# Performance work log

Measured on AMD Instinct MI355X. Metric: run time of the kernel, lower is better.

Reference implementation:

```python
import jax, jax.numpy as jnp
import numpy as np
from jax import lax

B = 32      # point clouds per batch
P = 1024    # points per cloud (equal-sized, contiguous in batch vector)
K = 20      # kNN neighbors (includes self, as in PyG knn)
N = B * P


def _w(key, fan_in, fan_out):
    return jax.random.normal(key, (fan_in, fan_out), dtype=jnp.float32) / np.sqrt(fan_in)


def setup_inputs() -> dict:
    key = jax.random.key(0)
    ks = jax.random.split(key, 12)
    return {
        "pos": jax.random.normal(ks[0], (N, 3), dtype=jnp.float32),
        "batch": jnp.repeat(jnp.arange(B, dtype=jnp.int32), P),
        # conv1 MLP([6,64,64]): Linear(6,64)+BN+ReLU, Linear(64,64) plain
        "conv1_W1": _w(ks[1], 6, 64),
        "conv1_b1": jnp.zeros((64,), jnp.float32),
        "conv1_bn_scale": jnp.ones((64,), jnp.float32),   # BN eval folded affine
        "conv1_bn_bias": jnp.zeros((64,), jnp.float32),
        "conv1_W2": _w(ks[2], 64, 64),
        "conv1_b2": jnp.zeros((64,), jnp.float32),
        # conv2 MLP([128,128]): single plain Linear(128,128)
        "conv2_W": _w(ks[3], 128, 128),
        "conv2_b": jnp.zeros((128,), jnp.float32),
        # lin: Linear(64+128, 128)
        "lin_W": _w(ks[4], 192, 128),
        "lin_b": jnp.zeros((128,), jnp.float32),
    }


def _edge_conv(x, mlp_fn):
    # x: [B, P, d]. Dynamic kNN in feature space per cloud, edge MLP, max-aggregate.
    sq = jnp.sum(x * x, axis=-1)                                  # [B,P]
    dist = sq[:, :, None] - 2.0 * jnp.einsum('bpd,bqd->bpq', x, x) + sq[:, None, :]
    _, idx = lax.top_k(-dist, K)                                  # [B,P,K] nearest (incl. self)
    x_j = jax.vmap(lambda xb, ib: xb[ib])(x, idx)                 # [B,P,K,d] gather neighbors
    x_i = jnp.broadcast_to(x[:, :, None, :], x_j.shape)
    e = jnp.concatenate([x_i, x_j - x_i], axis=-1)                # [B,P,K,2d]
    return jnp.max(mlp_fn(e), axis=2)                             # max aggregation -> [B,P,out]


def reference(pos, batch, conv1_W1, conv1_b1, conv1_bn_scale, conv1_bn_bias,
              conv1_W2, conv1_b2, conv2_W, conv2_b, lin_W, lin_b):
    x = pos.reshape(B, P, 3)

    def mlp1(e):
        h = e @ conv1_W1 + conv1_b1
        h = jax.nn.relu(h * conv1_bn_scale + conv1_bn_bias)       # BN(eval) + ReLU
        return h @ conv1_W2 + conv1_b2                            # plain last layer

    def mlp2(e):
        return e @ conv2_W + conv2_b                              # plain single layer

    x1 = _edge_conv(x, mlp1)                                      # [B,P,64]
    x2 = _edge_conv(x1, mlp2)                                     # [B,P,128]
    h = jnp.concatenate([x1, x2], axis=-1) @ lin_W + lin_b        # [B,P,128]
    # global_max_pool over each cloud via batch ids
    out = jax.ops.segment_max(h.reshape(N, 128), batch, num_segments=B)
    return out                                                    # [B,128]
```

## Files before the change

### kernel.cpp

```cpp
#include <hip/hip_runtime.h>
#include <math.h>

#define NPTS 32768
#define NB 32
#define PP 1024
#define KK 20

using bf16x8 = __attribute__((ext_vector_type(8))) short;
using f32x4 = __attribute__((ext_vector_type(4))) float;

constexpr size_t OFF_X1 = 0;
constexpr size_t OFF_IDX = OFF_X1 + (size_t)NPTS * 64 * 4;
constexpr size_t OFF_U = OFF_IDX + (size_t)NPTS * KK * 4;
constexpr size_t OFF_V = OFF_U + (size_t)NPTS * 128 * 4;
constexpr size_t OFF_X2 = OFF_V + (size_t)NPTS * 128 * 4;
constexpr size_t OFF_H = OFF_X2 + (size_t)NPTS * 128 * 4;
constexpr size_t OFF_PART = OFF_H + (size_t)NPTS * 128 * 4;
constexpr size_t OFF_SQN = OFF_PART + (size_t)32 * 8 * 128 * 4;

__device__ __forceinline__ void topk_insert(unsigned (&l)[KK], unsigned key) {
#pragma unroll
  for (int j = KK - 1; j >= 1; --j) {
    unsigned r;
    asm("v_med3_u32 %0, %1, %2, %3" : "=v"(r) : "v"(key), "v"(l[j - 1]), "v"(l[j]));
    l[j] = r;
  }
  l[0] = key < l[0] ? key : l[0];
}

__device__ __forceinline__ unsigned pack_key(float dist, int q) {
  return (__float_as_uint(dist) & 0xFFFFFC00u) | (unsigned)q;
}

__device__ __forceinline__ void split_bf16(float x, short& hi, short& lo) {
  unsigned u = __float_as_uint(x);
  hi = (short)(u >> 16);
  float fh = __uint_as_float(u & 0xFFFF0000u);
  float r = x - fh;
  lo = (short)(__float_as_uint(r) >> 16);
}

template <int S>
__global__ __launch_bounds__(256) void knn_topk3(const float* __restrict__ x,
                                                 unsigned* __restrict__ pk) {
  constexpr int CH = PP / S;
  __shared__ __align__(16) float xs[1024];
  __shared__ __align__(16) float ys[1024];
  __shared__ __align__(16) float zs[1024];
  int bx = blockIdx.x;
  int s = bx % S;
  int tile = (bx / S) % (PP / 256);
  int b = bx / (S * (PP / 256));
  int tid = threadIdx.x;
  const float* xb = x + (size_t)b * PP * 3;

  for (int t = tid; t < 768; t += 256) {
    float4 v = ((const float4*)xb)[t];
    int e = 4 * t;
    float vals[4] = {v.x, v.y, v.z, v.w};
#pragma unroll
    for (int j = 0; j < 4; ++j) {
      int p = (e + j) / 3, d = (e + j) % 3;
      if (d == 0) xs[p] = vals[j];
      else if (d == 1) ys[p] = vals[j];
      else zs[p] = vals[j];
    }
  }
  __syncthreads();

  int i = tile * 256 + tid;
  float xi0 = xs[i], xi1 = ys[i], xi2 = zs[i];

  unsigned l[KK];
#pragma unroll
  for (int j = 0; j < KK; ++j) l[j] = 0xFFFFFFFFu;

  int q0 = s * CH;
  float4 qx = *(const float4*)&xs[q0];
  float4 qy = *(const float4*)&ys[q0];
  float4 qz = *(const float4*)&zs[q0];
  for (int c = 0; c < CH; c += 4) {
    int qm = (q0 + c + 4) & 1023;
    float4 nqx = *(const float4*)&xs[qm];
    float4 nqy = *(const float4*)&ys[qm];
    float4 nqz = *(const float4*)&zs[qm];
    float cx[4] = {qx.x, qx.y, qx.z, qx.w};
    float cy[4] = {qy.x, qy.y, qy.z, qy.w};
    float cz[4] = {qz.x, qz.y, qz.z, qz.w};
#pragma unroll
    for (int j = 0; j < 4; ++j) {
      float d0 = xi0 - cx[j], d1 = xi1 - cy[j], d2 = xi2 - cz[j];
      float dist = fmaf(d0, d0, fmaf(d1, d1, d2 * d2));
      topk_insert(l, pack_key(dist, q0 + c + j));
    }
    qx = nqx; qy = nqy; qz = nqz;
  }
  size_t base = ((size_t)b * PP + i) * S + s;
#pragma unroll
  for (int j = 0; j < KK; ++j) pk[base * KK + j] = l[j];
}

template <int S>
__global__ __launch_bounds__(256) void knn_merge(const unsigned* __restrict__ pk,
                                                 int* __restrict__ idx_out) {
  int p = blockIdx.x * 256 + threadIdx.x;
  const unsigned* g = pk + (size_t)p * S * KK;
  unsigned l[KK];
#pragma unroll
  for (int j = 0; j < KK; ++j) l[j] = g[j];
  for (int s = 1; s < S; ++s) {
    const unsigned* gs = g + s * KK;
#pragma unroll
    for (int j = 0; j < KK; ++j) topk_insert(l, gs[j]);
  }
#pragma unroll
  for (int j = 0; j < KK; ++j) idx_out[(size_t)p * KK + j] = (int)(l[j] & 1023u);
}

__global__ __launch_bounds__(256) void precompute1(const float* __restrict__ pos,
                                                   const float* __restrict__ W1,
                                                   const float* __restrict__ b1,
                                                   float* __restrict__ u1,
                                                   float* __restrict__ v1) {
  int gid = blockIdx.x * 256 + threadIdx.x;
  int i = gid >> 6, c = gid & 63;
  float p0 = pos[(size_t)i * 3 + 0], p1 = pos[(size_t)i * 3 + 1], p2 = pos[(size_t)i * 3 + 2];
  float a0 = W1[0 * 64 + c], a1 = W1[1 * 64 + c], a2 = W1[2 * 64 + c];
  float g0 = W1[3 * 64 + c], g1 = W1[4 * 64 + c], g2 = W1[5 * 64 + c];
  float v = fmaf(p0, g0, fmaf(p1, g1, p2 * g2));
  float u = b1[c];
  u = fmaf(p0, a0 - g0, u);
  u = fmaf(p1, a1 - g1, u);
  u = fmaf(p2, a2 - g2, u);
  u1[gid] = u;
  v1[gid] = v;
}

__global__ __launch_bounds__(256) void edge_conv1_mfma(
    const float* __restrict__ u1, const float* __restrict__ v1,
    const int* __restrict__ idx, const float* __restrict__ W2,
    const float* __restrict__ scale, const float* __restrict__ bias,
    const float* __restrict__ b2,
    short* __restrict__ x1h, short* __restrict__ x1l,
    float* __restrict__ sqn) {
  __shared__ float Cs[160 * 68];
  __shared__ int jt[160];
  __shared__ float xs[512];
  int tid = threadIdx.x;
  int p0 = blockIdx.x * 8;
  int b = p0 >> 10;
  if (tid < 160) {
    int e = tid;
    int i = p0 + e / 20;
    jt[e] = (b << 10) + idx[(size_t)i * KK + e % 20];
  }
  int w = tid >> 6, l = tid & 63, quad = l >> 4, lm = l & 15;
  int kq = quad * 8;
  float4 s00 = *(const float4*)(scale + kq);
  float4 s01 = *(const float4*)(scale + kq + 4);
  float4 s10 = *(const float4*)(scale + 32 + kq);
  float4 s11 = *(const float4*)(scale + 32 + kq + 4);
  float4 c00 = *(const float4*)(bias + kq);
  float4 c01 = *(const float4*)(bias + kq + 4);
  float4 c10 = *(const float4*)(bias + 32 + kq);
  float4 c11 = *(const float4*)(bias + 32 + kq + 4);
  bf16x8 Bh[4][2], Bl[4][2];
#pragma unroll
  for (int nt = 0; nt < 4; ++nt) {
#pragma unroll
    for (int ks = 0; ks < 2; ++ks) {
#pragma unroll
      for (int jj = 0; jj < 8; ++jj) {
        float wv = W2[(size_t)(ks * 32 + kq + jj) * 64 + nt * 16 + lm];
        short hi, lo;
        split_bf16(wv, hi, lo);
        Bh[nt][ks][jj] = hi;
        Bl[nt][ks][jj] = lo;
      }
    }
  }
  __syncthreads();

  for (int s = w; s < 10; s += 4) {
    f32x4 acc[4];
#pragma unroll
    for (int nt = 0; nt < 4; ++nt) acc[nt] = (f32x4){0.f, 0.f, 0.f, 0.f};
    int e = s * 16 + lm;
    int p = e / 20;
    int jrow = jt[e];
    const float* urow = u1 + (size_t)(p0 + p) * 64;
    const float* vrow = v1 + (size_t)jrow * 64;
#pragma unroll
    for (int ks = 0; ks < 2; ++ks) {
      int koff = ks * 32 + kq;
      float4 va = *(const float4*)(vrow + koff);
      float4 vb = *(const float4*)(vrow + koff + 4);
      float4 ua = *(const float4*)(urow + koff);
      float4 ub = *(const float4*)(urow + koff + 4);
      float4 sA = ks ? s10 : s00, sB = ks ? s11 : s01;
      float4 cA = ks ? c10 : c00, cB = ks ? c11 : c01;
      float hv[8];
      hv[0] = fmaxf(fmaf(ua.x + va.x, sA.x, cA.x), 0.f);
      hv[1] = fmaxf(fmaf(ua.y + va.y, sA.y, cA.y), 0.f);
      hv[2] = fmaxf(fmaf(ua.z + va.z, sA.z, cA.z), 0.f);
      hv[3] = fmaxf(fmaf(ua.w + va.w, sA.w, cA.w), 0.f);
      hv[4] = fmaxf(fmaf(ub.x + vb.x, sB.x, cB.x), 0.f);
      hv[5] = fmaxf(fmaf(ub.y + vb.y, sB.y, cB.y), 0.f);
      hv[6] = fmaxf(fmaf(ub.z + vb.z, sB.z, cB.z), 0.f);
      hv[7] = fmaxf(fmaf(ub.w + vb.w, sB.w, cB.w), 0.f);
      bf16x8 Ah, Al;
#pragma unroll
      for (int jj = 0; jj < 8; ++jj) {
        short hi, lo;
        split_bf16(hv[jj], hi, lo);
        Ah[jj] = hi;
        Al[jj] = lo;
      }
#pragma unroll
      for (int nt = 0; nt < 4; ++nt) {
        acc[nt] = __builtin_amdgcn_mfma_f32_16x16x32_bf16(Ah, Bh[nt][ks], acc[nt], 0, 0, 0);
        acc[nt] = __builtin_amdgcn_mfma_f32_16x16x32_bf16(Al, Bh[nt][ks], acc[nt], 0, 0, 0);
        acc[nt] = __builtin_amdgcn_mfma_f32_16x16x32_bf16(Ah, Bl[nt][ks], acc[nt], 0, 0, 0);
      }
    }
#pragma unroll
    for (int nt = 0; nt < 4; ++nt) {
#pragma unroll
      for (int r = 0; r < 4; ++r) {
        Cs[(size_t)(s * 16 + quad * 4 + r) * 68 + nt * 16 + lm] = acc[nt][r];
      }
    }
  }
  __syncthreads();
  for (int o = tid; o < 512; o += 256) {
    int p = o >> 6, c = o & 63;
    float m = -__builtin_inff();
    for (int k = 0; k < KK; ++k) m = fmaxf(m, Cs[(size_t)(p * 20 + k) * 68 + c]);
    m += b2[c];
    size_t gi = (size_t)(p0 + p) * 64 + c;
    short hi, lo;
    split_bf16(m, hi, lo);
    x1h[gi] = hi;
    x1l[gi] = lo;
    xs[o] = m;
  }
  __syncthreads();
  if (tid < 8) {
    float ss = 0.f;
    for (int c = 0; c < 64; ++c) {
      float v = xs[tid * 64 + c];
      ss = fmaf(v, v, ss);
    }
    sqn[p0 + tid] = ss;
  }
}

__global__ __launch_bounds__(256) void knn2_mfma(const short* __restrict__ x1h,
                                                 const short* __restrict__ x1l,
                                                 const float* __restrict__ sqn,
                                                 unsigned* __restrict__ pk) {
  __shared__ float sqs[1024];
  int bx = blockIdx.x;
  int s = bx & 1;
  int pb = bx >> 1;
  int p0 = pb * 64;
  int b = p0 >> 10;
  int tid = threadIdx.x;
  for (int t = tid; t < 1024; t += 256) sqs[t] = sqn[(size_t)b * PP + t];
  int w = tid >> 6, l = tid & 63, quad = l >> 4, lm = l & 15;
  size_t gi = (size_t)p0 + w * 16 + lm;
  bf16x8 Bh[2], Bl[2];
#pragma unroll
  for (int ks = 0; ks < 2; ++ks) {
    Bh[ks] = *(const bf16x8*)(x1h + gi * 64 + ks * 32 + quad * 8);
    Bl[ks] = *(const bf16x8*)(x1l + gi * 64 + ks * 32 + quad * 8);
  }
  float sqi = sqn[gi];
  __syncthreads();
  unsigned list[KK];
#pragma unroll
  for (int j = 0; j < KK; ++j) list[j] = 0xFFFFFFFFu;

  const size_t cbase = (size_t)b * PP;
  int m0 = s * 512;
  bf16x8 Ah[2], Al[2];
  {
    size_t ga = cbase + m0 + lm;
    Ah[0] = *(const bf16x8*)(x1h + ga * 64 + quad * 8);
    Al[0] = *(const bf16x8*)(x1l + ga * 64 + quad * 8);
    Ah[1] = *(const bf16x8*)(x1h + ga * 64 + 32 + quad * 8);
    Al[1] = *(const bf16x8*)(x1l + ga * 64 + 32 + quad * 8);
  }
  float sq0 = sqs[m0 + quad * 4 + 0];
  float sq1 = sqs[m0 + quad * 4 + 1];
  float sq2 = sqs[m0 + quad * 4 + 2];
  float sq3 = sqs[m0 + quad * 4 + 3];

  for (int it = 0; it < 32; ++it) {
    int m0n = (m0 + 16) & 1023;
    size_t gan = cbase + m0n + lm;
    bf16x8 Ahn0 = *(const bf16x8*)(x1h + gan * 64 + quad * 8);
    bf16x8 Aln0 = *(const bf16x8*)(x1l + gan * 64 + quad * 8);
    bf16x8 Ahn1 = *(const bf16x8*)(x1h + gan * 64 + 32 + quad * 8);
    bf16x8 Aln1 = *(const bf16x8*)(x1l + gan * 64 + 32 + quad * 8);
    float sqn0 = sqs[m0n + quad * 4 + 0];
    float sqn1 = sqs[m0n + quad * 4 + 1];
    float sqn2 = sqs[m0n + quad * 4 + 2];
    float sqn3 = sqs[m0n + quad * 4 + 3];

    f32x4 acc = (f32x4){0.f, 0.f, 0.f, 0.f};
    acc = __builtin_amdgcn_mfma_f32_16x16x32_bf16(Ah[0], Bh[0], acc, 0, 0, 0);
    acc = __builtin_amdgcn_mfma_f32_16x16x32_bf16(Al[0], Bh[0], acc, 0, 0, 0);
    acc = __builtin_amdgcn_mfma_f32_16x16x32_bf16(Ah[0], Bl[0], acc, 0, 0, 0);
    acc = __builtin_amdgcn_mfma_f32_16x16x32_bf16(Ah[1], Bh[1], acc, 0, 0, 0);
    acc = __builtin_amdgcn_mfma_f32_16x16x32_bf16(Al[1], Bh[1], acc, 0, 0, 0);
    acc = __builtin_amdgcn_mfma_f32_16x16x32_bf16(Ah[1], Bl[1], acc, 0, 0, 0);

    int qb = m0 + quad * 4;
    float d0 = fmaxf(0.f, fmaf(-2.f, acc[0], sqi + sq0));
    topk_insert(list, pack_key(d0, qb + 0));
    float d1 = fmaxf(0.f, fmaf(-2.f, acc[1], sqi + sq1));
    topk_insert(list, pack_key(d1, qb + 1));
    float d2 = fmaxf(0.f, fmaf(-2.f, acc[2], sqi + sq2));
    topk_insert(list, pack_key(d2, qb + 2));
    float d3 = fmaxf(0.f, fmaf(-2.f, acc[3], sqi + sq3));
    topk_insert(list, pack_key(d3, qb + 3));

    Ah[0] = Ahn0; Al[0] = Aln0; Ah[1] = Ahn1; Al[1] = Aln1;
    sq0 = sqn0; sq1 = sqn1; sq2 = sqn2; sq3 = sqn3;
    m0 += 16;
  }
  unsigned sub = s * 4 + quad;
  unsigned* dst = pk + ((size_t)gi * 8 + sub) * KK;
#pragma unroll
  for (int j = 0; j < KK; ++j) dst[j] = list[j];
}

__global__ __launch_bounds__(256) void pre2_mfma(const short* __restrict__ x1h,
                                                 const short* __restrict__ x1l,
                                                 const float* __restrict__ cW,
                                                 const float* __restrict__ cb,
                                                 float* __restrict__ u2,
                                                 float* __restrict__ v2) {
  constexpr int BS = 72;
  __shared__ short Bh[128 * BS];
  __shared__ short Bl[128 * BS];
  int tid = threadIdx.x;
  int nh = blockIdx.x & 1;
  int p0 = (blockIdx.x >> 1) * 64;
  for (int t = tid; t < 64 * 128; t += 256) {
    int k = t >> 7, n = t & 127;
    float wb_ = cW[(size_t)(64 + k) * 128 + n];
    float wv = nh ? wb_ : (cW[(size_t)k * 128 + n] - wb_);
    short hi, lo;
    split_bf16(wv, hi, lo);
    Bh[n * BS + k] = hi;
    Bl[n * BS + k] = lo;
  }
  __syncthreads();
  int w = tid >> 6, l = tid & 63, quad = l >> 4, lm = l & 15;
  int row = p0 + w * 16 + lm;
  f32x4 acc[8];
#pragma unroll
  for (int nt = 0; nt < 8; ++nt) acc[nt] = (f32x4){0.f, 0.f, 0.f, 0.f};
#pragma unroll
  for (int ks = 0; ks < 2; ++ks) {
    int kb = ks * 32 + quad * 8;
    bf16x8 Ah = *(const bf16x8*)(x1h + (size_t)row * 64 + kb);
    bf16x8 Al = *(const bf16x8*)(x1l + (size_t)row * 64 + kb);
#pragma unroll
    for (int nt = 0; nt < 8; ++nt) {
      bf16x8 Wh = *(const bf16x8*)(Bh + (nt * 16 + lm) * BS + kb);
      bf16x8 Wl = *(const bf16x8*)(Bl + (nt * 16 + lm) * BS + kb);
      acc[nt] = __builtin_amdgcn_mfma_f32_16x16x32_bf16(Ah, Wh, acc[nt], 0, 0, 0);
      acc[nt] = __builtin_amdgcn_mfma_f32_16x16x32_bf16(Al, Wh, acc[nt], 0, 0, 0);
      acc[nt] = __builtin_amdgcn_mfma_f32_16x16x32_bf16(Ah, Wl, acc[nt], 0, 0, 0);
    }
  }
  float* out = nh ? v2 : u2;
  int prow = p0 + w * 16 + quad * 4;
#pragma unroll
  for (int nt = 0; nt < 8; ++nt) {
    int col = nt * 16 + lm;
    float bias = nh ? 0.f : cb[col];
#pragma unroll
    for (int r = 0; r < 4; ++r)
      out[(size_t)(prow + r) * 128 + col] = acc[nt][r] + bias;
  }
}

__global__ __launch_bounds__(256) void gathermax2(const float* __restrict__ u2,
                                                  const float* __restrict__ v2,
                                                  const int* __restrict__ idx,
                                                  short* __restrict__ x2h,
                                                  short* __restrict__ x2l) {
  int gid = blockIdx.x * 256 + threadIdx.x;
  int i = gid >> 7, c = gid & 127;
  int b = i >> 10;
  const int* myidx = idx + (size_t)i * KK;
  float m = -__builtin_inff();
  for (int k = 0; k < KK; ++k) {
    int j = (b << 10) + myidx[k];
    m = fmaxf(m, v2[(size_t)j * 128 + c]);
  }
  float x = u2[gid] + m;
  short hi, lo;
  split_bf16(x, hi, lo);
  x2h[gid] = hi;
  x2l[gid] = lo;
}

__global__ __launch_bounds__(256) void lin_mfma(const short* __restrict__ x1h,
                                                const short* __restrict__ x1l,
                                                const short* __restrict__ x2h,
                                                const short* __restrict__ x2l,
                                                const float* __restrict__ LW,
                                                const float* __restrict__ lb,
                                                float* __restrict__ h) {
  constexpr int BS = 200;
  __shared__ short Bh[64 * BS];
  __shared__ short Bl[64 * BS];
  int tid = threadIdx.x;
  int nh = blockIdx.x & 1;
  int p0 = (blockIdx.x >> 1) * 64;
  for (int t = tid; t < 192 * 64; t += 256) {
    int k = t >> 6, n = t & 63;
    float wv = LW[(size_t)k * 128 + nh * 64 + n];
    short hi, lo;
    split_bf16(wv, hi, lo);
    Bh[n * BS + k] = hi;
    Bl[n * BS + k] = lo;
  }
  __syncthreads();
  int w = tid >> 6, l = tid & 63, quad = l >> 4, lm = l & 15;
  int row = p0 + w * 16 + lm;
  f32x4 acc[4];
#pragma unroll
  for (int nt = 0; nt < 4; ++nt) acc[nt] = (f32x4){0.f, 0.f, 0.f, 0.f};
#pragma unroll
  for (int ks = 0; ks < 6; ++ks) {
    int kb = ks * 32 + quad * 8;
    bf16x8 Ah, Al;
    if (ks < 2) {
      Ah = *(const bf16x8*)(x1h + (size_t)row * 64 + kb);
      Al = *(const bf16x8*)(x1l + (size_t)row * 64 + kb);
    } else {
      Ah = *(const bf16x8*)(x2h + (size_t)row * 128 + (kb - 64));
      Al = *(const bf16x8*)(x2l + (size_t)row * 128 + (kb - 64));
    }
#pragma unroll
    for (int nt = 0; nt < 4; ++nt) {
      bf16x8 Wh = *(const bf16x8*)(Bh + (nt * 16 + lm) * BS + kb);
      bf16x8 Wl = *(const bf16x8*)(Bl + (nt * 16 + lm) * BS + kb);
      acc[nt] = __builtin_amdgcn_mfma_f32_16x16x32_bf16(Ah, Wh, acc[nt], 0, 0, 0);
      acc[nt] = __builtin_amdgcn_mfma_f32_16x16x32_bf16(Al, Wh, acc[nt], 0, 0, 0);
      acc[nt] = __builtin_amdgcn_mfma_f32_16x16x32_bf16(Ah, Wl, acc[nt], 0, 0, 0);
    }
  }
  int prow = p0 + w * 16 + quad * 4;
#pragma unroll
  for (int nt = 0; nt < 4; ++nt) {
    int col = nh * 64 + nt * 16 + lm;
    float bias = lb[col];
#pragma unroll
    for (int r = 0; r < 4; ++r)
      h[(size_t)(prow + r) * 128 + col] = acc[nt][r] + bias;
  }
}

__global__ __launch_bounds__(128) void segmax_a(const float* __restrict__ h,
                                                float* __restrict__ part) {
  int b = blockIdx.x >> 3, chunk = blockIdx.x & 7;
  int c = threadIdx.x;
  float m = -__builtin_inff();
  for (int p = 0; p < 128; ++p) {
    size_t i = (size_t)b * PP + chunk * 128 + p;
    m = fmaxf(m, h[i * 128 + c]);
  }
  part[(size_t)blockIdx.x * 128 + c] = m;
}

__global__ __launch_bounds__(128) void segmax_b(const float* __restrict__ part,
                                                float* __restrict__ out) {
  int b = blockIdx.x;
  int c = threadIdx.x;
  float m = -__builtin_inff();
  for (int k = 0; k < 8; ++k) m = fmaxf(m, part[((size_t)b * 8 + k) * 128 + c]);
  out[(size_t)b * 128 + c] = m;
}

extern "C" void kernel_launch(void* const* d_in, const int* in_sizes, int n_in,
                              void* d_out, int out_size, void* d_ws, size_t ws_size,
                              hipStream_t stream) {
  const float* pos = (const float*)d_in[0];
  const float* W1 = (const float*)d_in[2];
  const float* b1 = (const float*)d_in[3];
  const float* bn_s = (const float*)d_in[4];
  const float* bn_b = (const float*)d_in[5];
  const float* W2 = (const float*)d_in[6];
  const float* b2 = (const float*)d_in[7];
  const float* cW = (const float*)d_in[8];
  const float* cb = (const float*)d_in[9];
  const float* LW = (const float*)d_in[10];
  const float* lb = (const float*)d_in[11];
  float* out = (float*)d_out;

  char* ws = (char*)d_ws;
  short* x1h = (short*)(ws + OFF_X1);
  short* x1l = (short*)(ws + OFF_X1 + (size_t)NPTS * 64 * 2);
  int* idx = (int*)(ws + OFF_IDX);
  float* u1 = (float*)(ws + OFF_U);
  float* v1 = (float*)(ws + OFF_V);
  float* u2 = (float*)(ws + OFF_U);
  float* v2 = (float*)(ws + OFF_V);
  short* x2h = (short*)(ws + OFF_X2);
  short* x2l = (short*)(ws + OFF_X2 + (size_t)NPTS * 128 * 2);
  float* hbuf = (float*)(ws + OFF_H);
  float* part = (float*)(ws + OFF_PART);
  float* sqn = (float*)(ws + OFF_SQN);
  unsigned* pk = (unsigned*)(ws + OFF_U);

  knn_topk3<4><<<NB * 4 * 4, 256, 0, stream>>>(pos, pk);
  knn_merge<4><<<NPTS / 256, 256, 0, stream>>>(pk, idx);
  precompute1<<<NPTS * 64 / 256, 256, 0, stream>>>(pos, W1, b1, u1, v1);
  edge_conv1_mfma<<<NPTS / 8, 256, 0, stream>>>(u1, v1, idx, W2, bn_s, bn_b, b2,
                                                x1h, x1l, sqn);
  knn2_mfma<<<NPTS / 64 * 2, 256, 0, stream>>>(x1h, x1l, sqn, pk);
  knn_merge<8><<<NPTS / 256, 256, 0, stream>>>(pk, idx);
  pre2_mfma<<<NPTS / 64 * 2, 256, 0, stream>>>(x1h, x1l, cW, cb, u2, v2);
  gathermax2<<<NPTS * 128 / 256, 256, 0, stream>>>(u2, v2, idx, x2h, x2l);
  lin_mfma<<<NPTS / 64 * 2, 256, 0, stream>>>(x1h, x1l, x2h, x2l, LW, lb, hbuf);
  segmax_a<<<NB * 8, 128, 0, stream>>>(hbuf, part);
  segmax_b<<<NB, 128, 0, stream>>>(part, out);
}
```

Before: 340.8 us.

## Interleave bf16 hi/lo feature planes per row and split first kNN finer

The separate hi and lo bf16 planes of x1 and x2 are merged into one interleaved buffer per row, so each row's hi and lo parts sit next to each other and share cache lines and DRAM pages. The first kNN kernel now splits each cloud's candidates 8 ways instead of 4, with a matching 8-way merge, to launch more blocks. Launch bounds with a minimum of 4 blocks per SM are added to the two kNN kernels to raise occupancy, which may cause register spills in the top-k insertion loops.

```diff
diff --git a/kernel.cpp b/kernel.cpp
--- a/kernel.cpp
+++ b/kernel.cpp
@@ -41,8 +41,8 @@
 }
 
 template <int S>
-__global__ __launch_bounds__(256) void knn_topk3(const float* __restrict__ x,
-                                                 unsigned* __restrict__ pk) {
+__global__ __launch_bounds__(256, 4) void knn_topk3(const float* __restrict__ x,
+                                                    unsigned* __restrict__ pk) {
   constexpr int CH = PP / S;
   __shared__ __align__(16) float xs[1024];
   __shared__ __align__(16) float ys[1024];
@@ -141,8 +141,7 @@
     const int* __restrict__ idx, const float* __restrict__ W2,
     const float* __restrict__ scale, const float* __restrict__ bias,
     const float* __restrict__ b2,
-    short* __restrict__ x1h, short* __restrict__ x1l,
-    float* __restrict__ sqn) {
+    short* __restrict__ x1hl, float* __restrict__ sqn) {
   __shared__ float Cs[160 * 68];
   __shared__ int jt[160];
   __shared__ float xs[512];
@@ -237,11 +236,11 @@
     float m = -__builtin_inff();
     for (int k = 0; k < KK; ++k) m = fmaxf(m, Cs[(size_t)(p * 20 + k) * 68 + c]);
     m += b2[c];
-    size_t gi = (size_t)(p0 + p) * 64 + c;
+    size_t gi = (size_t)(p0 + p) * 128 + c;
     short hi, lo;
     split_bf16(m, hi, lo);
-    x1h[gi] = hi;
-    x1l[gi] = lo;
+    x1hl[gi] = hi;
+    x1hl[gi + 64] = lo;
     xs[o] = m;
   }
   __syncthreads();
@@ -255,10 +254,9 @@
   }
 }
 
-__global__ __launch_bounds__(256) void knn2_mfma(const short* __restrict__ x1h,
-                                                 const short* __restrict__ x1l,
-                                                 const float* __restrict__ sqn,
-                                                 unsigned* __restrict__ pk) {
+__global__ __launch_bounds__(256, 4) void knn2_mfma(const short* __restrict__ x1hl,
+                                                    const float* __restrict__ sqn,
+                                                    unsigned* __restrict__ pk) {
   __shared__ float sqs[1024];
   int bx = blockIdx.x;
   int s = bx & 1;
@@ -269,12 +267,11 @@
   for (int t = tid; t < 1024; t += 256) sqs[t] = sqn[(size_t)b * PP + t];
   int w = tid >> 6, l = tid & 63, quad = l >> 4, lm = l & 15;
   size_t gi = (size_t)p0 + w * 16 + lm;
-  bf16x8 Bh[2], Bl[2];
-#pragma unroll
-  for (int ks = 0; ks < 2; ++ks) {
-    Bh[ks] = *(const bf16x8*)(x1h + gi * 64 + ks * 32 + quad * 8);
-    Bl[ks] = *(const bf16x8*)(x1l + gi * 64 + ks * 32 + quad * 8);
-  }
+  const short* brow = x1hl + gi * 128 + quad * 8;
+  bf16x8 Bh0 = *(const bf16x8*)(brow);
+  bf16x8 Bl0 = *(const bf16x8*)(brow + 64);
+  bf16x8 Bh1 = *(const bf16x8*)(brow + 32);
+  bf16x8 Bl1 = *(const bf16x8*)(brow + 96);
   float sqi = sqn[gi];
   __syncthreads();
   unsigned list[KK];
@@ -283,14 +280,11 @@
 
   const size_t cbase = (size_t)b * PP;
   int m0 = s * 512;
-  bf16x8 Ah[2], Al[2];
-  {
-    size_t ga = cbase + m0 + lm;
-    Ah[0] = *(const bf16x8*)(x1h + ga * 64 + quad * 8);
-    Al[0] = *(const bf16x8*)(x1l + ga * 64 + quad * 8);
-    Ah[1] = *(const bf16x8*)(x1h + ga * 64 + 32 + quad * 8);
-    Al[1] = *(const bf16x8*)(x1l + ga * 64 + 32 + quad * 8);
-  }
+  const short* arow = x1hl + (cbase + m0 + lm) * 128 + quad * 8;
+  bf16x8 Ah0 = *(const bf16x8*)(arow);
+  bf16x8 Al0 = *(const bf16x8*)(arow + 64);
+  bf16x8 Ah1 = *(const bf16x8*)(arow + 32);
+  bf16x8 Al1 = *(const bf16x8*)(arow + 96);
   float sq0 = sqs[m0 + quad * 4 + 0];
   float sq1 = sqs[m0 + quad * 4 + 1];
   float sq2 = sqs[m0 + quad * 4 + 2];
@@ -298,23 +292,23 @@
 
   for (int it = 0; it < 32; ++it) {
     int m0n = (m0 + 16) & 1023;
-    size_t gan = cbase + m0n + lm;
-    bf16x8 Ahn0 = *(const bf16x8*)(x1h + gan * 64 + quad * 8);
-    bf16x8 Aln0 = *(const bf16x8*)(x1l + gan * 64 + quad * 8);
-    bf16x8 Ahn1 = *(const bf16x8*)(x1h + gan * 64 + 32 + quad * 8);
-    bf16x8 Aln1 = *(const bf16x8*)(x1l + gan * 64 + 32 + quad * 8);
-    float sqn0 = sqs[m0n + quad * 4 + 0];
-    float sqn1 = sqs[m0n + quad * 4 + 1];
-    float sqn2 = sqs[m0n + quad * 4 + 2];
-    float sqn3 = sqs[m0n + quad * 4 + 3];
+    const short* arn = x1hl + (cbase + m0n + lm) * 128 + quad * 8;
+    bf16x8 nAh0 = *(const bf16x8*)(arn);
+    bf16x8 nAl0 = *(const bf16x8*)(arn + 64);
+    bf16x8 nAh1 = *(const bf16x8*)(arn + 32);
+    bf16x8 nAl1 = *(const bf16x8*)(arn + 96);
+    float nsq0 = sqs[m0n + quad * 4 + 0];
+    float nsq1 = sqs[m0n + quad * 4 + 1];
+    float nsq2 = sqs[m0n + quad * 4 + 2];
+    float nsq3 = sqs[m0n + quad * 4 + 3];
 
     f32x4 acc = (f32x4){0.f, 0.f, 0.f, 0.f};
-    acc = __builtin_amdgcn_mfma_f32_16x16x32_bf16(Ah[0], Bh[0], acc, 0, 0, 0);
-    acc = __builtin_amdgcn_mfma_f32_16x16x32_bf16(Al[0], Bh[0], acc, 0, 0, 0);
-    acc = __builtin_amdgcn_mfma_f32_16x16x32_bf16(Ah[0], Bl[0], acc, 0, 0, 0);
-    acc = __builtin_amdgcn_mfma_f32_16x16x32_bf16(Ah[1], Bh[1], acc, 0, 0, 0);
-    acc = __builtin_amdgcn_mfma_f32_16x16x32_bf16(Al[1], Bh[1], acc, 0, 0, 0);
-    acc = __builtin_amdgcn_mfma_f32_16x16x32_bf16(Ah[1], Bl[1], acc, 0, 0, 0);
+    acc = __builtin_amdgcn_mfma_f32_16x16x32_bf16(Ah0, Bh0, acc, 0, 0, 0);
+    acc = __builtin_amdgcn_mfma_f32_16x16x32_bf16(Al0, Bh0, acc, 0, 0, 0);
+    acc = __builtin_amdgcn_mfma_f32_16x16x32_bf16(Ah0, Bl0, acc, 0, 0, 0);
+    acc = __builtin_amdgcn_mfma_f32_16x16x32_bf16(Ah1, Bh1, acc, 0, 0, 0);
+    acc = __builtin_amdgcn_mfma_f32_16x16x32_bf16(Al1, Bh1, acc, 0, 0, 0);
+    acc = __builtin_amdgcn_mfma_f32_16x16x32_bf16(Ah1, Bl1, acc, 0, 0, 0);
 
     int qb = m0 + quad * 4;
     float d0 = fmaxf(0.f, fmaf(-2.f, acc[0], sqi + sq0));
@@ -326,8 +320,8 @@
     float d3 = fmaxf(0.f, fmaf(-2.f, acc[3], sqi + sq3));
     topk_insert(list, pack_key(d3, qb + 3));
 
-    Ah[0] = Ahn0; Al[0] = Aln0; Ah[1] = Ahn1; Al[1] = Aln1;
-    sq0 = sqn0; sq1 = sqn1; sq2 = sqn2; sq3 = sqn3;
+    Ah0 = nAh0; Al0 = nAl0; Ah1 = nAh1; Al1 = nAl1;
+    sq0 = nsq0; sq1 = nsq1; sq2 = nsq2; sq3 = nsq3;
     m0 += 16;
   }
   unsigned sub = s * 4 + quad;
@@ -336,8 +330,7 @@
   for (int j = 0; j < KK; ++j) dst[j] = list[j];
 }
 
-__global__ __launch_bounds__(256) void pre2_mfma(const short* __restrict__ x1h,
-                                                 const short* __restrict__ x1l,
+__global__ __launch_bounds__(256) void pre2_mfma(const short* __restrict__ x1hl,
                                                  const float* __restrict__ cW,
                                                  const float* __restrict__ cb,
                                                  float* __restrict__ u2,
@@ -366,8 +359,8 @@
 #pragma unroll
   for (int ks = 0; ks < 2; ++ks) {
     int kb = ks * 32 + quad * 8;
-    bf16x8 Ah = *(const bf16x8*)(x1h + (size_t)row * 64 + kb);
-    bf16x8 Al = *(const bf16x8*)(x1l + (size_t)row * 64 + kb);
+    bf16x8 Ah = *(const bf16x8*)(x1hl + (size_t)row * 128 + kb);
+    bf16x8 Al = *(const bf16x8*)(x1hl + (size_t)row * 128 + 64 + kb);
 #pragma unroll
     for (int nt = 0; nt < 8; ++nt) {
       bf16x8 Wh = *(const bf16x8*)(Bh + (nt * 16 + lm) * BS + kb);
@@ -392,8 +385,7 @@
 __global__ __launch_bounds__(256) void gathermax2(const float* __restrict__ u2,
                                                   const float* __restrict__ v2,
                                                   const int* __restrict__ idx,
-                                                  short* __restrict__ x2h,
-                                                  short* __restrict__ x2l) {
+                                                  short* __restrict__ x2hl) {
   int gid = blockIdx.x * 256 + threadIdx.x;
   int i = gid >> 7, c = gid & 127;
   int b = i >> 10;
@@ -406,14 +398,12 @@
   float x = u2[gid] + m;
   short hi, lo;
   split_bf16(x, hi, lo);
-  x2h[gid] = hi;
-  x2l[gid] = lo;
-}
-
-__global__ __launch_bounds__(256) void lin_mfma(const short* __restrict__ x1h,
-                                                const short* __restrict__ x1l,
-                                                const short* __restrict__ x2h,
-                                                const short* __restrict__ x2l,
+  x2hl[(size_t)i * 256 + c] = hi;
+  x2hl[(size_t)i * 256 + 128 + c] = lo;
+}
+
+__global__ __launch_bounds__(256) void lin_mfma(const short* __restrict__ x1hl,
+                                                const short* __restrict__ x2hl,
                                                 const float* __restrict__ LW,
                                                 const float* __restrict__ lb,
                                                 float* __restrict__ h) {
@@ -442,11 +432,11 @@
     int kb = ks * 32 + quad * 8;
     bf16x8 Ah, Al;
     if (ks < 2) {
-      Ah = *(const bf16x8*)(x1h + (size_t)row * 64 + kb);
-      Al = *(const bf16x8*)(x1l + (size_t)row * 64 + kb);
+      Ah = *(const bf16x8*)(x1hl + (size_t)row * 128 + kb);
+      Al = *(const bf16x8*)(x1hl + (size_t)row * 128 + 64 + kb);
     } else {
-      Ah = *(const bf16x8*)(x2h + (size_t)row * 128 + (kb - 64));
-      Al = *(const bf16x8*)(x2l + (size_t)row * 128 + (kb - 64));
+      Ah = *(const bf16x8*)(x2hl + (size_t)row * 256 + (kb - 64));
+      Al = *(const bf16x8*)(x2hl + (size_t)row * 256 + 128 + (kb - 64));
     }
 #pragma unroll
     for (int nt = 0; nt < 4; ++nt) {
@@ -506,30 +496,28 @@
   float* out = (float*)d_out;
 
   char* ws = (char*)d_ws;
-  short* x1h = (short*)(ws + OFF_X1);
-  short* x1l = (short*)(ws + OFF_X1 + (size_t)NPTS * 64 * 2);
+  short* x1hl = (short*)(ws + OFF_X1);
   int* idx = (int*)(ws + OFF_IDX);
   float* u1 = (float*)(ws + OFF_U);
   float* v1 = (float*)(ws + OFF_V);
   float* u2 = (float*)(ws + OFF_U);
   float* v2 = (float*)(ws + OFF_V);
-  short* x2h = (short*)(ws + OFF_X2);
-  short* x2l = (short*)(ws + OFF_X2 + (size_t)NPTS * 128 * 2);
+  short* x2hl = (short*)(ws + OFF_X2);
   float* hbuf = (float*)(ws + OFF_H);
   float* part = (float*)(ws + OFF_PART);
   float* sqn = (float*)(ws + OFF_SQN);
   unsigned* pk = (unsigned*)(ws + OFF_U);
 
-  knn_topk3<4><<<NB * 4 * 4, 256, 0, stream>>>(pos, pk);
-  knn_merge<4><<<NPTS / 256, 256, 0, stream>>>(pk, idx);
+  knn_topk3<8><<<NB * 4 * 8, 256, 0, stream>>>(pos, pk);
+  knn_merge<8><<<NPTS / 256, 256, 0, stream>>>(pk, idx);
   precompute1<<<NPTS * 64 / 256, 256, 0, stream>>>(pos, W1, b1, u1, v1);
   edge_conv1_mfma<<<NPTS / 8, 256, 0, stream>>>(u1, v1, idx, W2, bn_s, bn_b, b2,
-                                                x1h, x1l, sqn);
-  knn2_mfma<<<NPTS / 64 * 2, 256, 0, stream>>>(x1h, x1l, sqn, pk);
+                                                x1hl, sqn);
+  knn2_mfma<<<NPTS / 64 * 2, 256, 0, stream>>>(x1hl, sqn, pk);
   knn_merge<8><<<NPTS / 256, 256, 0, stream>>>(pk, idx);
-  pre2_mfma<<<NPTS / 64 * 2, 256, 0, stream>>>(x1h, x1l, cW, cb, u2, v2);
-  gathermax2<<<NPTS * 128 / 256, 256, 0, stream>>>(u2, v2, idx, x2h, x2l);
-  lin_mfma<<<NPTS / 64 * 2, 256, 0, stream>>>(x1h, x1l, x2h, x2l, LW, lb, hbuf);
+  pre2_mfma<<<NPTS / 64 * 2, 256, 0, stream>>>(x1hl, cW, cb, u2, v2);
+  gathermax2<<<NPTS * 128 / 256, 256, 0, stream>>>(u2, v2, idx, x2hl);
+  lin_mfma<<<NPTS / 64 * 2, 256, 0, stream>>>(x1hl, x2hl, LW, lb, hbuf);
   segmax_a<<<NB * 8, 128, 0, stream>>>(hbuf, part);
   segmax_b<<<NB, 128, 0, stream>>>(part, out);
 }
```

Measured after the change: 344.6 us. Within noise of the previous version (+1.1%).
